# Kernel tuning notes

Measured on AMD Instinct MI355X. Metric: run time of the kernel, lower is better.

The kernel has to match this reference:

```python
import jax, jax.numpy as jnp
import numpy as np

NUM_HEADS = 16
D_MODEL = 1024
HEAD_DIM = D_MODEL // NUM_HEADS
B, S = 2, 2048


def setup_inputs() -> dict:
    key = jax.random.key(0)
    ks = jax.random.split(key, 11)
    scale = 1.0 / np.sqrt(D_MODEL)
    inp = {
        'query': jax.random.normal(ks[0], (B, S, D_MODEL), jnp.float32),
        'key': jax.random.normal(ks[1], (B, S, D_MODEL), jnp.float32),
        'value': jax.random.normal(ks[2], (B, S, D_MODEL), jnp.float32),
        'Wq': jax.random.normal(ks[3], (D_MODEL, D_MODEL), jnp.float32) * scale,
        'bq': jnp.zeros((D_MODEL,), jnp.float32),
        'Wk': jax.random.normal(ks[4], (D_MODEL, D_MODEL), jnp.float32) * scale,
        'bk': jnp.zeros((D_MODEL,), jnp.float32),
        'Wv': jax.random.normal(ks[5], (D_MODEL, D_MODEL), jnp.float32) * scale,
        'bv': jnp.zeros((D_MODEL,), jnp.float32),
        'Wo': jax.random.normal(ks[6], (D_MODEL, D_MODEL), jnp.float32) * scale,
        'bo': jnp.zeros((D_MODEL,), jnp.float32),
    }
    return inp


def reference(query, key, value, Wq, bq, Wk, bk, Wv, bv, Wo, bo):
    b, s, _ = query.shape
    # Linear projections (torch Linear: x @ W.T + b; here W stored as [in,out])
    Q = query @ Wq + bq
    K = key @ Wk + bk
    V = value @ Wv + bv
    # [B, H, S, Dh]
    Q = Q.reshape(b, s, NUM_HEADS, HEAD_DIM).transpose(0, 2, 1, 3)
    K = K.reshape(b, -1, NUM_HEADS, HEAD_DIM).transpose(0, 2, 1, 3)
    V = V.reshape(b, -1, NUM_HEADS, HEAD_DIM).transpose(0, 2, 1, 3)
    scores = jnp.einsum('bhqd,bhkd->bhqk', Q, K) / jnp.sqrt(jnp.float32(HEAD_DIM)).astype(Q.dtype)
    attn = jax.nn.softmax(scores, axis=-1)
    ctx = jnp.einsum('bhqk,bhkd->bhqd', attn, V)
    ctx = ctx.transpose(0, 2, 1, 3).reshape(b, s, D_MODEL)
    return ctx @ Wo + bo
```

## Files before the change

### kernel.cpp

```cpp
#include <hip/hip_runtime.h>
#include <hip/hip_bf16.h>
#include <math.h>

#define NUM_HEADS 16
#define D_MODEL 1024
#define HEAD_DIM 64
#define BATCH 2
#define SEQ 2048
#define M_TOTAL (BATCH*SEQ)

typedef __bf16 bf16;
typedef __bf16 bf16x2 __attribute__((ext_vector_type(2)));
typedef __bf16 bf16x4 __attribute__((ext_vector_type(4)));
typedef __bf16 bf16x8 __attribute__((ext_vector_type(8)));
typedef float  floatx4 __attribute__((ext_vector_type(4)));

#define CLSCALE 0.180336884f

__device__ __forceinline__ void async_copy16(const bf16* g, bf16* l) {
    __builtin_amdgcn_global_load_lds(
        (const __attribute__((address_space(1))) void*)g,
        (__attribute__((address_space(3))) void*)l, 16, 0, 0);
}

__global__ __launch_bounds__(256)
void convert_kernel(const float* __restrict__ Wq, const float* __restrict__ Wk,
                    const float* __restrict__ Wv, const float* __restrict__ Wo,
                    const float* __restrict__ q, const float* __restrict__ k,
                    const float* __restrict__ v,
                    bf16* __restrict__ Wt, bf16* __restrict__ Xb)
{
    const int blk = blockIdx.x;
    const int tid = threadIdx.x;
    if (blk < 256) {
        const int wi  = blk >> 6;
        const int sub = blk & 63;
        const int xb  = sub & 3;
        const int yb  = sub >> 2;
        const float* W = (wi == 0) ? Wq : (wi == 1) ? Wk : (wi == 2) ? Wv : Wo;
        bf16* dstM = Wt + (size_t)wi * D_MODEL * D_MODEL;
        const int n  = xb * 256 + tid;
        const int k0 = yb * 64;
        bf16* dst = dstM + (size_t)n * D_MODEL + k0;
        #pragma unroll
        for (int jc = 0; jc < 8; ++jc) {
            bf16x8 w;
            #pragma unroll
            for (int j = 0; j < 8; ++j)
                w[j] = (bf16)W[(size_t)(k0 + jc * 8 + j) * D_MODEL + n];
            *(bf16x8*)(dst + jc * 8) = w;
        }
    } else {
        const int rem   = blk - 256;
        const int plane = rem >> 11;
        const int xb    = rem & 2047;
        const float* X = (plane == 0) ? q : (plane == 1) ? k : v;
        bf16* dst = Xb + (size_t)plane * M_TOTAL * D_MODEL;
        size_t i = ((size_t)xb * 256 + tid) * 8;
        const float4 u = *(const float4*)(X + i);
        const float4 w = *(const float4*)(X + i + 4);
        bf16x8 o;
        o[0] = (bf16)u.x; o[1] = (bf16)u.y; o[2] = (bf16)u.z; o[3] = (bf16)u.w;
        o[4] = (bf16)w.x; o[5] = (bf16)w.y; o[6] = (bf16)w.z; o[7] = (bf16)w.w;
        *(bf16x8*)(dst + i) = o;
    }
}

__global__ __launch_bounds__(256)
void proj_kernel(const bf16* __restrict__ Xb, const bf16* __restrict__ Wt,
                 const float* __restrict__ bq, const float* __restrict__ bk,
                 const float* __restrict__ bv,
                 bf16* __restrict__ Qo, bf16* __restrict__ Ko, bf16* __restrict__ Vto)
{
    const int which = blockIdx.z;
    const bf16* X     = Xb + (size_t)which * M_TOTAL * D_MODEL;
    const bf16* Wm    = Wt + (size_t)which * D_MODEL * D_MODEL;
    const float* bias = (which == 0) ? bq : (which == 1) ? bk : bv;

    const int tileM = blockIdx.y * 128;
    const int tileN = blockIdx.x * 128;
    const int tid  = threadIdx.x;
    const int lane = tid & 63;
    const int wave = tid >> 6;
    const int quad = lane >> 4;
    const int l16  = lane & 15;

    __shared__ bf16 sA[128 * 32];
    __shared__ bf16 sB[128 * 32];

    floatx4 acc[4][4];
    const floatx4 z4 = {0.0f, 0.0f, 0.0f, 0.0f};
    #pragma unroll
    for (int i = 0; i < 4; i++)
        #pragma unroll
        for (int j = 0; j < 4; j++) acc[i][j] = z4;

    const int wm = (wave >> 1) * 64;
    const int wn = (wave & 1) * 64;

    const int c0   = wave * 64 + lane;
    const int row0 = c0 >> 2, col0 = (c0 & 3) * 8;
    const int c1   = c0 + 256;
    const int row1 = c1 >> 2, col1 = (c1 & 3) * 8;
    bf16* ldsA0 = sA + (size_t)(wave * 64) * 8;
    bf16* ldsA1 = sA + (size_t)(256 + wave * 64) * 8;
    bf16* ldsB0 = sB + (size_t)(wave * 64) * 8;
    bf16* ldsB1 = sB + (size_t)(256 + wave * 64) * 8;

    for (int k0 = 0; k0 < D_MODEL; k0 += 32) {
        __syncthreads();
        async_copy16(X  + (size_t)(tileM + row0) * D_MODEL + k0 + col0, ldsA0);
        async_copy16(X  + (size_t)(tileM + row1) * D_MODEL + k0 + col1, ldsA1);
        async_copy16(Wm + (size_t)(tileN + row0) * D_MODEL + k0 + col0, ldsB0);
        async_copy16(Wm + (size_t)(tileN + row1) * D_MODEL + k0 + col1, ldsB1);
        __syncthreads();

        bf16x8 af[4], bfr[4];
        #pragma unroll
        for (int i = 0; i < 4; i++) af[i]  = *(const bf16x8*)&sA[(wm + i * 16 + l16) * 32 + quad * 8];
        #pragma unroll
        for (int j = 0; j < 4; j++) bfr[j] = *(const bf16x8*)&sB[(wn + j * 16 + l16) * 32 + quad * 8];
        if (which != 2) {
            #pragma unroll
            for (int i = 0; i < 4; i++)
                #pragma unroll
                for (int j = 0; j < 4; j++)
                    acc[i][j] = __builtin_amdgcn_mfma_f32_16x16x32_bf16(af[i], bfr[j], acc[i][j], 0, 0, 0);
        } else {
            #pragma unroll
            for (int i = 0; i < 4; i++)
                #pragma unroll
                for (int j = 0; j < 4; j++)
                    acc[i][j] = __builtin_amdgcn_mfma_f32_16x16x32_bf16(bfr[i], af[j], acc[i][j], 0, 0, 0);
        }
    }

    if (which != 2) {
        bf16* out = (which == 0) ? Qo : Ko;
        const float oscale = (which == 0) ? CLSCALE : 1.0f;
        #pragma unroll
        for (int i = 0; i < 4; i++) {
            int mbase = tileM + wm + i * 16 + quad * 4;
            #pragma unroll
            for (int j = 0; j < 4; j++) {
                int n = tileN + wn + j * 16 + l16;
                float bb = bias[n];
                int h = n >> 6, d = n & 63;
                #pragma unroll
                for (int r = 0; r < 4; r++) {
                    int mm = mbase + r;
                    int b = mm >> 11, s = mm & 2047;
                    out[(((size_t)(b * NUM_HEADS + h)) * SEQ + s) * HEAD_DIM + d] =
                        (bf16)((acc[i][j][r] + bb) * oscale);
                }
            }
        }
    } else {
        #pragma unroll
        for (int i = 0; i < 4; i++) {
            #pragma unroll
            for (int r = 0; r < 4; r++) {
                int n = tileN + wn + i * 16 + quad * 4 + r;
                float bb = bias[n];
                int h = n >> 6, d = n & 63;
                #pragma unroll
                for (int j = 0; j < 4; j++) {
                    int m = tileM + wm + j * 16 + l16;
                    int b = m >> 11, s = m & 2047;
                    Vto[(((size_t)(b * NUM_HEADS + h)) * HEAD_DIM + d) * SEQ + s] =
                        (bf16)(acc[i][j][r] + bb);
                }
            }
        }
    }
}

__global__ __launch_bounds__(256)
void attn_kernel(const bf16* __restrict__ Q, const bf16* __restrict__ K,
                 const bf16* __restrict__ Vt, bf16* __restrict__ Ctx)
{
    const int lin    = blockIdx.x;
    const int xcd    = lin & 7;
    const int rest   = lin >> 3;
    const int superg = rest >> 5;
    const int qi     = rest & 31;
    const int bh     = superg * 8 + xcd;
    const int b      = bh >> 4, h = bh & 15;
    const int q0     = qi * 64;

    const int tid = threadIdx.x;
    const int lane = tid & 63;
    const int wave = tid >> 6;
    const int quad = lane >> 4;
    const int l16  = lane & 15;

    __shared__ bf16 sQP[64][72];
    __shared__ bf16 sK[64 * 64];
    __shared__ bf16 sVt[64 * 64];

    const bf16* Qb  = Q  + ((size_t)bh * SEQ + q0) * HEAD_DIM;
    const bf16* Kb  = K  + (size_t)bh * SEQ * HEAD_DIM;
    const bf16* Vtb = Vt + (size_t)bh * HEAD_DIM * SEQ;

    #pragma unroll
    for (int it = 0; it < 2; ++it) {
        int g   = tid + it * 256;
        int row = g >> 3;
        int c   = (g & 7) * 8;
        *(bf16x8*)&sQP[row][c] = *(const bf16x8*)(Qb + (size_t)row * HEAD_DIM + c);
    }
    __syncthreads();

    const int m0 = wave * 16;
    bf16x8 bQ[2];
    bQ[0] = *(const bf16x8*)&sQP[m0 + l16][quad * 8];
    bQ[1] = *(const bf16x8*)&sQP[m0 + l16][32 + quad * 8];

    floatx4 o[4];
    const floatx4 z4 = {0.0f, 0.0f, 0.0f, 0.0f};
    #pragma unroll
    for (int t = 0; t < 4; t++) o[t] = z4;
    floatx4 lpart = z4;

    const int xs = l16 & 7;
    const int cho0 = ((quad)     ^ xs) * 8;
    const int cho1 = ((4 + quad) ^ xs) * 8;

    for (int kt = 0; kt < SEQ / 64; ++kt) {
        __syncthreads();
        #pragma unroll
        for (int it = 0; it < 2; ++it) {
            int c    = tid + it * 256;
            int row  = c >> 3;
            int scol = ((c & 7) ^ (row & 7)) * 8;
            async_copy16(Kb  + (size_t)(kt * 64 + row) * HEAD_DIM + scol,
                         sK + (size_t)c * 8);
            async_copy16(Vtb + (size_t)row * SEQ + kt * 64 + scol,
                         sVt + (size_t)c * 8);
        }
        __syncthreads();

        floatx4 sc[4];
        #pragma unroll
        for (int t = 0; t < 4; t++) {
            const int ra = (t * 16 + l16) * 64;
            bf16x8 a0 = *(const bf16x8*)&sK[ra + cho0];
            bf16x8 a1 = *(const bf16x8*)&sK[ra + cho1];
            floatx4 z = z4;
            z = __builtin_amdgcn_mfma_f32_16x16x32_bf16(a0, bQ[0], z, 0, 0, 0);
            z = __builtin_amdgcn_mfma_f32_16x16x32_bf16(a1, bQ[1], z, 0, 0, 0);
            sc[t] = z;
        }

        #pragma unroll
        for (int t = 0; t < 4; t++)
            #pragma unroll
            for (int r = 0; r < 4; r++)
                sc[t][r] = exp2f(sc[t][r]);
        lpart += sc[0] + sc[1] + sc[2] + sc[3];

        #pragma unroll
        for (int t = 0; t < 4; t++) {
            bf16x4 pk;
            #pragma unroll
            for (int r = 0; r < 4; r++) pk[r] = (bf16)sc[t][r];
            *(bf16x4*)&sQP[m0 + l16][t * 16 + quad * 4] = pk;
        }

        bf16x8 bP0 = *(const bf16x8*)&sQP[m0 + l16][quad * 8];
        bf16x8 bP1 = *(const bf16x8*)&sQP[m0 + l16][32 + quad * 8];

        #pragma unroll
        for (int dt = 0; dt < 4; dt++) {
            const int ra = (dt * 16 + l16) * 64;
            bf16x8 a0 = *(const bf16x8*)&sVt[ra + cho0];
            bf16x8 a1 = *(const bf16x8*)&sVt[ra + cho1];
            o[dt] = __builtin_amdgcn_mfma_f32_16x16x32_bf16(a0, bP0, o[dt], 0, 0, 0);
            o[dt] = __builtin_amdgcn_mfma_f32_16x16x32_bf16(a1, bP1, o[dt], 0, 0, 0);
        }
    }

    float rs = (lpart[0] + lpart[1]) + (lpart[2] + lpart[3]);
    rs += __shfl_xor(rs, 16, 64);
    rs += __shfl_xor(rs, 32, 64);
    float inv = 1.0f / rs;

    int qq = q0 + m0 + l16;
    size_t base = ((size_t)b * SEQ + qq) * D_MODEL + h * HEAD_DIM;
    #pragma unroll
    for (int dt = 0; dt < 4; dt++) {
        bf16x4 w;
        #pragma unroll
        for (int r = 0; r < 4; r++) w[r] = (bf16)(o[dt][r] * inv);
        *(bf16x4*)&Ctx[base + dt * 16 + quad * 4] = w;
    }
}

__global__ __launch_bounds__(256)
void out_proj_kernel(const bf16* __restrict__ A, const bf16* __restrict__ Wto,
                     const float* __restrict__ bias, float* __restrict__ Out)
{
    const int tileM = blockIdx.y * 64;
    const int tileN = blockIdx.x * 128;
    const int tid  = threadIdx.x;
    const int lane = tid & 63;
    const int wave = tid >> 6;
    const int quad = lane >> 4;
    const int l16  = lane & 15;

    __shared__ bf16 sA[64 * 32];
    __shared__ bf16 sB[128 * 32];

    floatx4 acc[2][4];
    const floatx4 z4 = {0.0f, 0.0f, 0.0f, 0.0f};
    #pragma unroll
    for (int i = 0; i < 2; i++)
        #pragma unroll
        for (int j = 0; j < 4; j++) acc[i][j] = z4;

    const int wm = (wave >> 1) * 32;
    const int wn = (wave & 1) * 64;

    const int c0   = wave * 64 + lane;
    const int row0 = c0 >> 2, col0 = (c0 & 3) * 8;
    const int c1   = c0 + 256;
    const int row1 = c1 >> 2, col1 = (c1 & 3) * 8;
    bf16* ldsA0 = sA + (size_t)(wave * 64) * 8;
    bf16* ldsB0 = sB + (size_t)(wave * 64) * 8;
    bf16* ldsB1 = sB + (size_t)(256 + wave * 64) * 8;

    for (int k0 = 0; k0 < D_MODEL; k0 += 32) {
        __syncthreads();
        async_copy16(A   + (size_t)(tileM + row0) * D_MODEL + k0 + col0, ldsA0);
        async_copy16(Wto + (size_t)(tileN + row0) * D_MODEL + k0 + col0, ldsB0);
        async_copy16(Wto + (size_t)(tileN + row1) * D_MODEL + k0 + col1, ldsB1);
        __syncthreads();

        bf16x8 af[2], bfr[4];
        #pragma unroll
        for (int i = 0; i < 2; i++) af[i]  = *(const bf16x8*)&sA[(wm + i * 16 + l16) * 32 + quad * 8];
        #pragma unroll
        for (int j = 0; j < 4; j++) bfr[j] = *(const bf16x8*)&sB[(wn + j * 16 + l16) * 32 + quad * 8];
        #pragma unroll
        for (int i = 0; i < 2; i++)
            #pragma unroll
            for (int j = 0; j < 4; j++)
                acc[i][j] = __builtin_amdgcn_mfma_f32_16x16x32_bf16(af[i], bfr[j], acc[i][j], 0, 0, 0);
    }

    #pragma unroll
    for (int i = 0; i < 2; i++) {
        int mbase = tileM + wm + i * 16 + quad * 4;
        #pragma unroll
        for (int j = 0; j < 4; j++) {
            int n = tileN + wn + j * 16 + l16;
            float bb = bias[n];
            #pragma unroll
            for (int r = 0; r < 4; r++)
                Out[(size_t)(mbase + r) * D_MODEL + n] = acc[i][j][r] + bb;
        }
    }
}

extern "C" void kernel_launch(void* const* d_in, const int* in_sizes, int n_in,
                              void* d_out, int out_size, void* d_ws, size_t ws_size,
                              hipStream_t stream)
{
    const float* q  = (const float*)d_in[0];
    const float* k  = (const float*)d_in[1];
    const float* v  = (const float*)d_in[2];
    const float* Wq = (const float*)d_in[3];
    const float* bq = (const float*)d_in[4];
    const float* Wk = (const float*)d_in[5];
    const float* bk = (const float*)d_in[6];
    const float* Wv = (const float*)d_in[7];
    const float* bv = (const float*)d_in[8];
    const float* Wo = (const float*)d_in[9];
    const float* bo = (const float*)d_in[10];
    float* out = (float*)d_out;

    const size_t PLANE = (size_t)M_TOTAL * D_MODEL;
    bf16* Qb = (bf16*)d_ws;
    bf16* Kb = Qb + PLANE;
    bf16* Vt = Kb + PLANE;
    bf16* Cb = Vt + PLANE;
    bf16* Wt = Cb + PLANE;
    bf16* Xb = Wt + 4 * (size_t)D_MODEL * D_MODEL;

    convert_kernel<<<dim3(6400), 256, 0, stream>>>(Wq, Wk, Wv, Wo, q, k, v, Wt, Xb);
    proj_kernel<<<dim3(8, 32, 3), 256, 0, stream>>>(Xb, Wt, bq, bk, bv, Qb, Kb, Vt);
    attn_kernel<<<dim3(1024), 256, 0, stream>>>(Qb, Kb, Vt, Cb);
    out_proj_kernel<<<dim3(8, 64), 256, 0, stream>>>(Cb, Wt + 3 * (size_t)D_MODEL * D_MODEL, bo, out);
}
```

Measured before the change: 258.2 us.

## Use 32x32 MFMA with split-K waves in attention and XCD-aware GEMM tile mapping

The attention kernel moves from 16x16x32 MFMA tiles, where each wave owns 16 query rows, to 32x32x16 MFMA tiles. Waves are split into two query halves and two key halves, and the partial outputs and row sums are reduced through shared memory at the end. The aim is fewer LDS reads per FLOP and a higher MFMA rate, at the cost of an extra reduction, more accumulator registers and extra syncs. The projection and output GEMMs also remap a 1D grid so that blocks on the same XCD share M tiles, for better L2 locality.

```diff
diff --git a/kernel.cpp b/kernel.cpp
--- a/kernel.cpp
+++ b/kernel.cpp
@@ -13,7 +13,8 @@
 typedef __bf16 bf16x2 __attribute__((ext_vector_type(2)));
 typedef __bf16 bf16x4 __attribute__((ext_vector_type(4)));
 typedef __bf16 bf16x8 __attribute__((ext_vector_type(8)));
-typedef float  floatx4 __attribute__((ext_vector_type(4)));
+typedef float  floatx4  __attribute__((ext_vector_type(4)));
+typedef float  floatx16 __attribute__((ext_vector_type(16)));
 
 #define CLSCALE 0.180336884f
 
@@ -72,13 +73,20 @@
                  const float* __restrict__ bv,
                  bf16* __restrict__ Qo, bf16* __restrict__ Ko, bf16* __restrict__ Vto)
 {
-    const int which = blockIdx.z;
+    const int lin  = blockIdx.x;
+    const int xcd  = lin & 7;
+    const int idx  = lin >> 3;
+    const int nt   = idx & 7;
+    const int t2   = idx >> 3;
+    const int mloc = t2 & 3;
+    const int which= t2 >> 2;
+    const int tileM = (xcd * 4 + mloc) * 128;
+    const int tileN = nt * 128;
+
     const bf16* X     = Xb + (size_t)which * M_TOTAL * D_MODEL;
     const bf16* Wm    = Wt + (size_t)which * D_MODEL * D_MODEL;
     const float* bias = (which == 0) ? bq : (which == 1) ? bk : bv;
 
-    const int tileM = blockIdx.y * 128;
-    const int tileN = blockIdx.x * 128;
     const int tid  = threadIdx.x;
     const int lane = tid & 63;
     const int wave = tid >> 6;
@@ -188,15 +196,20 @@
     const int b      = bh >> 4, h = bh & 15;
     const int q0     = qi * 64;
 
-    const int tid = threadIdx.x;
+    const int tid  = threadIdx.x;
     const int lane = tid & 63;
     const int wave = tid >> 6;
-    const int quad = lane >> 4;
-    const int l16  = lane & 15;
+    const int half = lane >> 5;
+    const int m31  = lane & 31;
+    const int xs   = m31 & 7;
+
+    const int qsub  = wave & 1;
+    const int kjsub = wave >> 1;
 
     __shared__ bf16 sQP[64][72];
     __shared__ bf16 sK[64 * 64];
     __shared__ bf16 sVt[64 * 64];
+    __shared__ float sL[64];
 
     const bf16* Qb  = Q  + ((size_t)bh * SEQ + q0) * HEAD_DIM;
     const bf16* Kb  = K  + (size_t)bh * SEQ * HEAD_DIM;
@@ -211,20 +224,15 @@
     }
     __syncthreads();
 
-    const int m0 = wave * 16;
-    bf16x8 bQ[2];
-    bQ[0] = *(const bf16x8*)&sQP[m0 + l16][quad * 8];
-    bQ[1] = *(const bf16x8*)&sQP[m0 + l16][32 + quad * 8];
-
-    floatx4 o[4];
-    const floatx4 z4 = {0.0f, 0.0f, 0.0f, 0.0f};
-    #pragma unroll
-    for (int t = 0; t < 4; t++) o[t] = z4;
-    floatx4 lpart = z4;
-
-    const int xs = l16 & 7;
-    const int cho0 = ((quad)     ^ xs) * 8;
-    const int cho1 = ((4 + quad) ^ xs) * 8;
+    bf16x8 bQ[4];
+    #pragma unroll
+    for (int s = 0; s < 4; s++)
+        bQ[s] = *(const bf16x8*)&sQP[qsub * 32 + m31][s * 16 + half * 8];
+
+    floatx16 o0, o1;
+    #pragma unroll
+    for (int r = 0; r < 16; r++) { o0[r] = 0.0f; o1[r] = 0.0f; }
+    float lp = 0.0f;
 
     for (int kt = 0; kt < SEQ / 64; ++kt) {
         __syncthreads();
@@ -240,59 +248,81 @@
         }
         __syncthreads();
 
-        floatx4 sc[4];
-        #pragma unroll
-        for (int t = 0; t < 4; t++) {
-            const int ra = (t * 16 + l16) * 64;
-            bf16x8 a0 = *(const bf16x8*)&sK[ra + cho0];
-            bf16x8 a1 = *(const bf16x8*)&sK[ra + cho1];
-            floatx4 z = z4;
-            z = __builtin_amdgcn_mfma_f32_16x16x32_bf16(a0, bQ[0], z, 0, 0, 0);
-            z = __builtin_amdgcn_mfma_f32_16x16x32_bf16(a1, bQ[1], z, 0, 0, 0);
-            sc[t] = z;
-        }
-
-        #pragma unroll
-        for (int t = 0; t < 4; t++)
-            #pragma unroll
-            for (int r = 0; r < 4; r++)
-                sc[t][r] = exp2f(sc[t][r]);
-        lpart += sc[0] + sc[1] + sc[2] + sc[3];
-
-        #pragma unroll
-        for (int t = 0; t < 4; t++) {
+        floatx16 sc;
+        #pragma unroll
+        for (int r = 0; r < 16; r++) sc[r] = 0.0f;
+        #pragma unroll
+        for (int s = 0; s < 4; s++) {
+            bf16x8 a = *(const bf16x8*)&sK[(kjsub * 32 + m31) * 64 + (((2 * s + half) ^ xs) * 8)];
+            sc = __builtin_amdgcn_mfma_f32_32x32x16_bf16(a, bQ[s], sc, 0, 0, 0);
+        }
+
+        #pragma unroll
+        for (int r = 0; r < 16; r++) sc[r] = exp2f(sc[r]);
+        float ls = 0.0f;
+        #pragma unroll
+        for (int r = 0; r < 16; r++) ls += sc[r];
+        lp += ls;
+
+        #pragma unroll
+        for (int rg = 0; rg < 4; rg++) {
             bf16x4 pk;
             #pragma unroll
-            for (int r = 0; r < 4; r++) pk[r] = (bf16)sc[t][r];
-            *(bf16x4*)&sQP[m0 + l16][t * 16 + quad * 4] = pk;
-        }
-
-        bf16x8 bP0 = *(const bf16x8*)&sQP[m0 + l16][quad * 8];
-        bf16x8 bP1 = *(const bf16x8*)&sQP[m0 + l16][32 + quad * 8];
-
-        #pragma unroll
-        for (int dt = 0; dt < 4; dt++) {
-            const int ra = (dt * 16 + l16) * 64;
-            bf16x8 a0 = *(const bf16x8*)&sVt[ra + cho0];
-            bf16x8 a1 = *(const bf16x8*)&sVt[ra + cho1];
-            o[dt] = __builtin_amdgcn_mfma_f32_16x16x32_bf16(a0, bP0, o[dt], 0, 0, 0);
-            o[dt] = __builtin_amdgcn_mfma_f32_16x16x32_bf16(a1, bP1, o[dt], 0, 0, 0);
-        }
-    }
-
-    float rs = (lpart[0] + lpart[1]) + (lpart[2] + lpart[3]);
-    rs += __shfl_xor(rs, 16, 64);
-    rs += __shfl_xor(rs, 32, 64);
-    float inv = 1.0f / rs;
-
-    int qq = q0 + m0 + l16;
-    size_t base = ((size_t)b * SEQ + qq) * D_MODEL + h * HEAD_DIM;
-    #pragma unroll
-    for (int dt = 0; dt < 4; dt++) {
-        bf16x4 w;
-        #pragma unroll
-        for (int r = 0; r < 4; r++) w[r] = (bf16)(o[dt][r] * inv);
-        *(bf16x4*)&Ctx[base + dt * 16 + quad * 4] = w;
+            for (int i = 0; i < 4; i++) pk[i] = (bf16)sc[rg * 4 + i];
+            *(bf16x4*)&sQP[qsub * 32 + m31][kjsub * 32 + rg * 8 + half * 4] = pk;
+        }
+
+        bf16x8 bP[2];
+        #pragma unroll
+        for (int s = 0; s < 2; s++)
+            bP[s] = *(const bf16x8*)&sQP[qsub * 32 + m31][kjsub * 32 + s * 16 + half * 8];
+
+        #pragma unroll
+        for (int s = 0; s < 2; s++) {
+            int ch = ((4 * kjsub + 2 * s + half) ^ xs) * 8;
+            bf16x8 a0 = *(const bf16x8*)&sVt[(size_t)m31 * 64 + ch];
+            bf16x8 a1 = *(const bf16x8*)&sVt[(size_t)(32 + m31) * 64 + ch];
+            o0 = __builtin_amdgcn_mfma_f32_32x32x16_bf16(a0, bP[s], o0, 0, 0, 0);
+            o1 = __builtin_amdgcn_mfma_f32_32x32x16_bf16(a1, bP[s], o1, 0, 0, 0);
+        }
+    }
+
+    lp += __shfl_xor(lp, 32, 64);
+
+    __syncthreads();
+    float* fO = (qsub == 0) ? (float*)sK : (float*)sVt;
+    if (kjsub == 1) {
+        #pragma unroll
+        for (int r = 0; r < 16; r++) {
+            fO[r * 64 + lane]        = o0[r];
+            fO[1024 + r * 64 + lane] = o1[r];
+        }
+        if (half == 0) sL[qsub * 32 + m31] = lp;
+    }
+    __syncthreads();
+    if (kjsub == 0) {
+        #pragma unroll
+        for (int r = 0; r < 16; r++) {
+            o0[r] += fO[r * 64 + lane];
+            o1[r] += fO[1024 + r * 64 + lane];
+        }
+        float denom = lp + sL[qsub * 32 + m31];
+        float inv = 1.0f / denom;
+
+        int q = q0 + qsub * 32 + m31;
+        size_t base = ((size_t)b * SEQ + q) * D_MODEL + h * HEAD_DIM;
+        #pragma unroll
+        for (int rg = 0; rg < 4; rg++) {
+            int d0 = rg * 8 + half * 4;
+            bf16x4 w0, w1;
+            #pragma unroll
+            for (int i = 0; i < 4; i++) {
+                w0[i] = (bf16)(o0[rg * 4 + i] * inv);
+                w1[i] = (bf16)(o1[rg * 4 + i] * inv);
+            }
+            *(bf16x4*)&Ctx[base + d0]      = w0;
+            *(bf16x4*)&Ctx[base + 32 + d0] = w1;
+        }
     }
 }
 
@@ -300,8 +330,14 @@
 void out_proj_kernel(const bf16* __restrict__ A, const bf16* __restrict__ Wto,
                      const float* __restrict__ bias, float* __restrict__ Out)
 {
-    const int tileM = blockIdx.y * 64;
-    const int tileN = blockIdx.x * 128;
+    const int lin  = blockIdx.x;
+    const int xcd  = lin & 7;
+    const int idx  = lin >> 3;
+    const int nt   = idx & 7;
+    const int mloc = idx >> 3;
+    const int tileM = (xcd * 8 + mloc) * 64;
+    const int tileN = nt * 128;
+
     const int tid  = threadIdx.x;
     const int lane = tid & 63;
     const int wave = tid >> 6;
@@ -388,7 +424,7 @@
     bf16* Xb = Wt + 4 * (size_t)D_MODEL * D_MODEL;
 
     convert_kernel<<<dim3(6400), 256, 0, stream>>>(Wq, Wk, Wv, Wo, q, k, v, Wt, Xb);
-    proj_kernel<<<dim3(8, 32, 3), 256, 0, stream>>>(Xb, Wt, bq, bk, bv, Qb, Kb, Vt);
+    proj_kernel<<<dim3(768), 256, 0, stream>>>(Xb, Wt, bq, bk, bv, Qb, Kb, Vt);
     attn_kernel<<<dim3(1024), 256, 0, stream>>>(Qb, Kb, Vt, Cb);
-    out_proj_kernel<<<dim3(8, 64), 256, 0, stream>>>(Cb, Wt + 3 * (size_t)D_MODEL * D_MODEL, bo, out);
-}
+    out_proj_kernel<<<dim3(512), 256, 0, stream>>>(Cb, Wt + 3 * (size_t)D_MODEL * D_MODEL, bo, out);
+}
```

Measured after the change: 247.4 us. -4.2%, faster.
